# Performance work log

Hardware: AMD Instinct MI355X
Metric: run time of the kernel (lower is better)

Reference implementation:

```python
import math
import jax, jax.numpy as jnp
import numpy as np

# ---------------- static structure (mirrors CG_woFilter_cuda + MyBatchNormWeightMM) ----------------
LMAX = 4
TAUS = [16, 16, 16, 16, 16]          # t_F: input channels per degree l
T_O  = [16, 16, 16, 16, 16]          # output channels per degree l after weight matmul
BN_EPS = 1e-5

# all (l, l1, l2) triples with l2 <= l1 <= lmax and |l1-l2| <= l <= min(l1+l2, lmax), sorted by (l,l1,l2)
TRIPLES = sorted([(l, l1, l2)
                  for l1 in range(LMAX + 1)
                  for l2 in range(l1 + 1)
                  for l in range(l1 - l2, min(l1 + l2, LMAX) + 1)])

T_FF = [0] * (LMAX + 1)              # t_FF[l] = sum over triples of taus[l1]*taus[l2]
for (l, l1, l2) in TRIPLES:
    T_FF[l] += TAUS[l1] * TAUS[l2]

def _cg_coef(j1, m1, j2, m2, j, m):
    """Clebsch-Gordan coefficient <j1 m1 j2 m2 | j m> (Condon-Shortley)."""
    if m1 + m2 != m:
        return 0.0
    f = math.factorial
    if j < abs(j1 - j2) or j > j1 + j2:
        return 0.0
    pref = math.sqrt((2 * j + 1) * f(j + j1 - j2) * f(j - j1 + j2) * f(j1 + j2 - j) / f(j1 + j2 + j + 1))
    pref *= math.sqrt(f(j + m) * f(j - m) * f(j1 - m1) * f(j1 + m1) * f(j2 - m2) * f(j2 + m2))
    s = 0.0
    for k in range(0, j1 + j2 - j + 1):
        if (j1 - m1 - k) < 0 or (j2 + m2 - k) < 0 or (j - j2 + m1 + k) < 0 or (j - j1 - m2 + k) < 0:
            continue
        s += ((-1.0) ** k) / (f(k) * f(j1 + j2 - j - k) * f(j1 - m1 - k)
                              * f(j2 + m2 - k) * f(j - j2 + m1 + k) * f(j - j1 - m2 + k))
    return pref * s

def _cg_matrix(l, l1, l2):
    C = np.zeros((2 * l + 1, 2 * l1 + 1, 2 * l2 + 1), dtype=np.float32)
    for m in range(-l, l + 1):
        for m1 in range(-l1, l1 + 1):
            m2 = m - m1
            if -l2 <= m2 <= l2:
                C[m + l, m1 + l1, m2 + l2] = _cg_coef(l1, m1, l2, m2, l, m)
    return C

CG_MATS = {t: jnp.asarray(_cg_matrix(*t)) for t in TRIPLES}

M_IN = sum(TAUS[l] * (2 * l + 1) for l in range(LMAX + 1))      # 400
W_LEN = sum(T_FF[l] * T_O[l] for l in range(LMAX + 1))          # 172032


def setup_inputs() -> dict:
    key = jax.random.key(0)
    k1, k2 = jax.random.split(key)
    B = 256
    Fs = jax.random.normal(k1, (B, M_IN, 2), dtype=jnp.float32)
    W = jax.random.normal(k2, (W_LEN, 2), dtype=jnp.float32) * 0.05
    return {"Fs": Fs, "W": W}


def reference(Fs, W):
    B = Fs.shape[0]
    # split input into per-degree blocks: F_l [B, tau, 2l+1, 2]
    Fl, off = [], 0
    for l in range(LMAX + 1):
        n = TAUS[l] * (2 * l + 1)
        Fl.append(Fs[:, off:off + n, :].reshape(B, TAUS[l], 2 * l + 1, 2))
        off += n
    # sparse CG tensor product: per-triple complex outer product contracted with CG coefs
    frags = [[] for _ in range(LMAX + 1)]
    for (l, l1, l2) in TRIPLES:
        C = CG_MATS[(l, l1, l2)]                     # [2l+1, 2l1+1, 2l2+1]
        a, b = Fl[l1], Fl[l2]
        ar, ai = a[..., 0], a[..., 1]
        br, bi = b[..., 0], b[..., 1]
        rr = jnp.einsum('bip,bjq,mpq->bijm', ar, br, C)
        ii = jnp.einsum('bip,bjq,mpq->bijm', ai, bi, C)
        ri = jnp.einsum('bip,bjq,mpq->bijm', ar, bi, C)
        ir = jnp.einsum('bip,bjq,mpq->bijm', ai, br, C)
        fr = (rr - ii).reshape(B, -1, 2 * l + 1)     # channels flattened as c1*tau2 + c2 (t_offsets order)
        fi = (ri + ir).reshape(B, -1, 2 * l + 1)
        frags[l].append(jnp.stack([fr, fi], axis=-1))
    # per-degree fragment batchnorm + complex weight matmul (FN_WMM)
    outs, woff = [], 0
    for l in range(LMAX + 1):
        FF = jnp.concatenate(frags[l], axis=1)       # [B, t_FF, 2l+1, 2]
        var = jnp.mean(jnp.sum(FF * FF, axis=-1), axis=(0, 2))      # per-channel mean |z|^2
        FFn = FF / (jnp.sqrt(var)[None, :, None, None] + BN_EPS)
        n = T_FF[l] * T_O[l]
        Wl = W[woff:woff + n].reshape(T_O[l], T_FF[l], 2)
        woff += n
        wr, wi = Wl[..., 0], Wl[..., 1]
        xr, xi = FFn[..., 0], FFn[..., 1]
        yr = jnp.einsum('oc,bcm->bom', wr, xr) - jnp.einsum('oc,bcm->bom', wi, xi)
        yi = jnp.einsum('oc,bcm->bom', wr, xi) + jnp.einsum('oc,bcm->bom', wi, xr)
        outs.append(jnp.stack([yr, yi], axis=-1).reshape(B, T_O[l] * (2 * l + 1), 2))
    return jnp.concatenate(outs, axis=1)             # [B, sum t_O[l]*(2l+1), 2] = [B, 400, 2]
```

## Files before the change

kernel.cpp:

```cpp
#include <hip/hip_runtime.h>
#include <math.h>

#define NTRI 42
#define NCH  10752
#define B_SZ 256
#define AH_PL 172032

typedef float    f32x4 __attribute__((ext_vector_type(4)));
typedef _Float16 half8 __attribute__((ext_vector_type(8)));
typedef _Float16 half4 __attribute__((ext_vector_type(4)));
typedef _Float16 f16x2 __attribute__((ext_vector_type(2)));

constexpr int CT_L [NTRI]={0,0,0,0,0, 1,1,1,1,1,1,1,1, 2,2,2,2,2,2,2,2,2,2, 3,3,3,3,3,3,3,3,3,3, 4,4,4,4,4,4,4,4,4};
constexpr int CT_L1[NTRI]={0,1,2,3,4, 1,1,2,2,3,3,4,4, 1,2,2,2,3,3,3,4,4,4, 2,2,3,3,3,3,4,4,4,4, 2,3,3,3,4,4,4,4,4};
constexpr int CT_L2[NTRI]={0,1,2,3,4, 0,1,1,2,2,3,3,4, 1,0,1,2,1,2,3,2,3,4, 1,2,0,1,2,3,1,2,3,4, 2,1,2,3,0,1,2,3,4};
constexpr int CT_T [NTRI]={0,1,2,3,4, 0,1,2,3,4,5,6,7, 0,1,2,3,4,5,6,7,8,9, 0,1,2,3,4,5,6,7,8,9, 0,1,2,3,4,5,6,7,8};

constexpr int KL_t[5]    ={1280,2048,2560,2560,2304};
constexpr int GBASE_t[5] ={0,1280,3328,5888,8448};
constexpr int ROFF_t[5]  ={0,16,64,144,256};
constexpr int NM_t[5]    ={1,3,5,7,9};
constexpr int FFB_t[5]   ={0,327680,1900544,5177344,9764864};
#define FF_TOT 15073280
constexpr int PL_t[5]    ={0,5,29,79,149};
#define PART_PL 4096
#define PART_TOT (230*PART_PL)

__device__ const int   dCTL[NTRI]={0,0,0,0,0, 1,1,1,1,1,1,1,1, 2,2,2,2,2,2,2,2,2,2, 3,3,3,3,3,3,3,3,3,3, 4,4,4,4,4,4,4,4,4};
__device__ const int   dCTT[NTRI]={0,1,2,3,4, 0,1,2,3,4,5,6,7, 0,1,2,3,4,5,6,7,8,9, 0,1,2,3,4,5,6,7,8,9, 0,1,2,3,4,5,6,7,8};
__device__ const int   dK[5]   ={1280,2048,2560,2560,2304};
__device__ const int   dWOFF[5]={0,20480,53248,94208,135168};
__device__ const int   dNM[5]  ={1,3,5,7,9};
__device__ const int   dFFB[5] ={0,327680,1900544,5177344,9764864};
__device__ const int   dPL[5]  ={0,5,29,79,149};
__device__ const int   dGB[5]  ={0,1280,3328,5888,8448};
__device__ const int   dROFF[5]={0,16,64,144,256};
__device__ const int   dNT[5]  ={5,8,10,10,9};
__device__ const float dINV[5] ={1.f/256.f,1.f/768.f,1.f/1280.f,1.f/1792.f,1.f/2304.f};

__device__ float  g_varsum[NCH];
__device__ __align__(16) f16x2  g_ff[FF_TOT];
__device__ __align__(16) f16x2  g_ah[2*AH_PL];
__device__ float2 g_part[PART_TOT];

constexpr double cfact(int n){ double r=1.0; for(int i=2;i<=n;i++) r*=(double)i; return r; }
constexpr double csqrt_(double v){ double x = v>1.0? v:1.0; for(int i=0;i<80;i++) x = 0.5*(x+v/x); return x; }
constexpr double ccg(int j1,int m1,int j2,int m2,int j,int m){
    if(m1+m2!=m) return 0.0;
    double pref = csqrt_((2.0*j+1.0)*cfact(j+j1-j2)*cfact(j-j1+j2)*cfact(j1+j2-j)/cfact(j1+j2+j+1));
    pref *= csqrt_(cfact(j+m)*cfact(j-m)*cfact(j1-m1)*cfact(j1+m1)*cfact(j2-m2)*cfact(j2+m2));
    double s=0.0;
    for(int k=0;k<=j1+j2-j;k++){
        int a=j1-m1-k, bb=j2+m2-k, c=j-j2+m1+k, d=j-j1-m2+k;
        if(a<0||bb<0||c<0||d<0) continue;
        double term = 1.0/(cfact(k)*cfact(j1+j2-j-k)*cfact(a)*cfact(bb)*cfact(c)*cfact(d));
        s += (k&1)? -term : term;
    }
    return pref*s;
}
struct CG81 { float a[81]; };
constexpr CG81 makecg(int l,int l1,int l2){
    CG81 t{};
    const int n1=2*l1+1;
    for(int mi=0;mi<2*l+1;mi++)
        for(int p=0;p<n1;p++){
            const int m=mi-l, m1=p-l1, m2=m-m1;
            if(m2>=-l2 && m2<=l2) t.a[mi*n1+p]=(float)ccg(l1,m1,l2,m2,l,m);
        }
    return t;
}
template<int TR> struct CGC { static constexpr CG81 t = makecg(CT_L[TR],CT_L1[TR],CT_L2[TR]); };

template<int TR>
__device__ __forceinline__ void cg_pair(const float2* __restrict__ sF,
                                        int i, int j0,
                                        float2* __restrict__ ff0,
                                        float2* __restrict__ ff1){
    constexpr int L=CT_L[TR], L1=CT_L1[TR], L2=CT_L2[TR];
    constexpr int N1=2*L1+1, N2=2*L2+1, NM=2*L+1;
    float2 A[N1], B0[N2], B1[N2];
    #pragma unroll
    for(int p=0;p<N1;p++) A[p]=sF[ROFF_t[L1]+i*N1+p];
    #pragma unroll
    for(int q=0;q<N2;q++) B0[q]=sF[ROFF_t[L2]+j0*N2+q];
    #pragma unroll
    for(int q=0;q<N2;q++) B1[q]=sF[ROFF_t[L2]+(j0+1)*N2+q];
    #pragma unroll
    for(int mi=0;mi<NM;mi++){
        float aR0=0.f, aI0=0.f, aR1=0.f, aI1=0.f;
        const int pLo = (mi-L+L1-L2) > 0 ? (mi-L+L1-L2) : 0;
        const int pHi = (mi-L+L1+L2) < 2*L1 ? (mi-L+L1+L2) : 2*L1;
        #pragma unroll
        for(int p=0;p<N1;p++){
            if(p>=pLo && p<=pHi){
                const float c = CGC<TR>::t.a[mi*N1+p];
                if(c != 0.f){
                    const int q = mi - L - p + L1 + L2;
                    const float2 a=A[p];
                    const float2 b0=B0[q], b1=B1[q];
                    aR0 = fmaf(c, a.x*b0.x - a.y*b0.y, aR0);
                    aI0 = fmaf(c, a.x*b0.y + a.y*b0.x, aI0);
                    aR1 = fmaf(c, a.x*b1.x - a.y*b1.y, aR1);
                    aI1 = fmaf(c, a.x*b1.y + a.y*b1.x, aI1);
                }
            }
        }
        ff0[mi]=make_float2(aR0,aI0);
        ff1[mi]=make_float2(aR1,aI1);
    }
}

template<int TR>
__device__ __forceinline__ void cg_one(const float2* __restrict__ sF, int bq, int t){
    constexpr int L=CT_L[TR], NM=2*L+1, T=CT_T[TR], K=KL_t[L];
    constexpr int NMK=NM*K;
    const int half = t>>7, tt = t&127;
    const int ch0 = tt*2;
    const int i = ch0>>4, j0 = ch0&15;
    float n20=0.f, n21=0.f;
    #pragma unroll
    for(int b4=0;b4<4;b4++){
        const int slab = half*4+b4;
        const int b = bq*8 + slab;
        float2 ff0[NM], ff1[NM];
        cg_pair<TR>(sF + slab*400, i, j0, ff0, ff1);
        const int base = FFB_t[L] + b*NMK + T*256 + ch0;
        #pragma unroll
        for(int m=0;m<NM;m++){
            n20 = fmaf(ff0[m].x,ff0[m].x,n20); n20 = fmaf(ff0[m].y,ff0[m].y,n20);
            n21 = fmaf(ff1[m].x,ff1[m].x,n21); n21 = fmaf(ff1[m].y,ff1[m].y,n21);
            half4 h;
            h[0]=(_Float16)ff0[m].x; h[1]=(_Float16)ff0[m].y;
            h[2]=(_Float16)ff1[m].x; h[3]=(_Float16)ff1[m].y;
            *reinterpret_cast<half4*>(g_ff + base + m*K) = h;
        }
    }
    atomicAdd(&g_varsum[GBASE_t[L] + T*256 + ch0    ], n20);
    atomicAdd(&g_varsum[GBASE_t[L] + T*256 + ch0 + 1], n21);
}

template<int TR>
__device__ __forceinline__ void cg_disp(int tr, const float2* sF, int bq, int t){
    if constexpr (TR < NTRI){
        if(tr==TR) cg_one<TR>(sF,bq,t);
        else       cg_disp<TR+1>(tr,sF,bq,t);
    }
}

__global__ void __launch_bounds__(256) k_cg(const float2* __restrict__ Fs){
    __shared__ float4 sF4[1600];
    const int bq=blockIdx.y, t=threadIdx.x;
    const float4* __restrict__ F4 = reinterpret_cast<const float4*>(Fs) + bq*1600;
    #pragma unroll
    for(int k=0;k<6;k++) sF4[t + k*256] = F4[t + k*256];
    if(t<64) sF4[t+1536] = F4[t+1536];
    __syncthreads();
    cg_disp<0>(blockIdx.x, reinterpret_cast<const float2*>(sF4), bq, t);
}

__global__ void __launch_bounds__(256) k_wn(const float2* __restrict__ W2){
    const int tr=blockIdx.x, t=threadIdx.x;
    const int l=dCTL[tr], T=dCTT[tr], K=dK[l];
    const float s = g_varsum[dGB[l] + T*256 + t];
    const float invv = 1.f/(sqrtf(s*dINV[l])+1e-5f);
    const int base = dWOFF[l] + T*256 + t;
    #pragma unroll 4
    for(int o=0;o<16;o++){
        const float2 w = W2[base + o*K];
        f16x2 hr, hi;
        hr.x=(_Float16)( w.x*invv); hr.y=(_Float16)(-w.y*invv);
        hi.x=(_Float16)( w.y*invv); hi.y=(_Float16)( w.x*invv);
        g_ah[base + o*K]         = hr;
        g_ah[AH_PL + base + o*K] = hi;
    }
}

__global__ void __launch_bounds__(256) k_mm(){
    const int j=blockIdx.x;
    const int wv=threadIdx.x>>6, lane=threadIdx.x&63;
    const int slot=blockIdx.y*4+wv;
    const int bgA=slot, bgB=slot+8;
    const int l=(j<5)?0:(j<29)?1:(j<79)?2:(j<149)?3:4;
    const int nm=dNM[l];
    const int loc=j-dPL[l];
    const int T=loc/nm, m=loc-T*nm;
    const int K=dK[l];
    const int l15=lane&15, kg=lane>>4;
    const half8* __restrict__ Arp = reinterpret_cast<const half8*>(g_ah + dWOFF[l] + l15*K + T*256 + kg*4);
    const half8* __restrict__ Aip = reinterpret_cast<const half8*>(g_ah + AH_PL + dWOFF[l] + l15*K + T*256 + kg*4);
    const half8* __restrict__ XpA = reinterpret_cast<const half8*>(g_ff + dFFB[l] + (bgA*16+l15)*(nm*K) + m*K + T*256 + kg*4);
    const half8* __restrict__ XpB = reinterpret_cast<const half8*>(g_ff + dFFB[l] + (bgB*16+l15)*(nm*K) + m*K + T*256 + kg*4);
    f32x4 arA={0.f,0.f,0.f,0.f}, aiA={0.f,0.f,0.f,0.f};
    f32x4 arB={0.f,0.f,0.f,0.f}, aiB={0.f,0.f,0.f,0.f};
    #pragma unroll
    for(int ks=0; ks<16; ks++){
        const half8 Ar = Arp[ks*4];
        const half8 Ai = Aip[ks*4];
        const half8 BA = XpA[ks*4];
        const half8 BB = XpB[ks*4];
        arA = __builtin_amdgcn_mfma_f32_16x16x32_f16(Ar, BA, arA, 0,0,0);
        aiA = __builtin_amdgcn_mfma_f32_16x16x32_f16(Ai, BA, aiA, 0,0,0);
        arB = __builtin_amdgcn_mfma_f32_16x16x32_f16(Ar, BB, arB, 0,0,0);
        aiB = __builtin_amdgcn_mfma_f32_16x16x32_f16(Ai, BB, aiB, 0,0,0);
    }
    float2* __restrict__ ppA = g_part + j*PART_PL + bgA*256;
    float2* __restrict__ ppB = g_part + j*PART_PL + bgB*256;
    #pragma unroll
    for(int r=0;r<4;r++){
        ppA[(kg*4+r)*16 + l15] = make_float2(arA[r], aiA[r]);
        ppB[(kg*4+r)*16 + l15] = make_float2(arB[r], aiB[r]);
    }
}

__global__ void __launch_bounds__(448) k_red(float2* __restrict__ out){
    const int b=blockIdx.x, r=threadIdx.x;
    if(r>=400) return;
    const int l = (r<16)?0:(r<64)?1:(r<144)?2:(r<256)?3:4;
    const int om = r - dROFF[l];
    const int nm = dNM[l];
    const int o = om/nm, m = om - o*nm;
    const float2* __restrict__ pp = g_part + (dPL[l]+m)*PART_PL + (b>>4)*256 + o*16 + (b&15);
    float2 s=make_float2(0.f,0.f);
    const int nt=dNT[l];
    for(int T=0;T<nt;T++){
        const float2 v = pp[T*nm*PART_PL];
        s.x+=v.x; s.y+=v.y;
    }
    out[b*400+r]=s;
}

extern "C" void kernel_launch(void* const* d_in, const int* in_sizes, int n_in,
                              void* d_out, int out_size, void* d_ws, size_t ws_size,
                              hipStream_t stream){
    const float2* Fs = (const float2*)d_in[0];
    const float2* W  = (const float2*)d_in[1];
    float2* out = (float2*)d_out;

    void* dvs=nullptr;
    hipGetSymbolAddress(&dvs, HIP_SYMBOL(g_varsum));
    hipMemsetAsync(dvs, 0, NCH*sizeof(float), stream);

    k_cg <<<dim3(NTRI,32), 256, 0, stream>>>(Fs);
    k_wn <<<dim3(NTRI),    256, 0, stream>>>(W);
    k_mm <<<dim3(230,2),   256, 0, stream>>>();
    k_red<<<dim3(B_SZ),    448, 0, stream>>>(out);
}
```

Measured before the change: 116.5 us.

## Register-block CG products over four j-channels and drop varsum memset

Each thread in the CG kernel now computes four output channels (one i, four consecutive j) for two batch slabs, instead of two channels for four slabs. This reuses the A vector and the CG coefficient products across four B vectors and writes half8 stores. The hipMemsetAsync of the variance accumulator is removed; k_wn now zeroes each entry after reading it, which relies on the buffer starting at zero on the first call. The trade-offs are more register pressure from the B arrays and a non-unrolled slab loop.

```diff
diff --git a/kernel.cpp b/kernel.cpp
--- a/kernel.cpp
+++ b/kernel.cpp
@@ -72,71 +72,63 @@
 template<int TR> struct CGC { static constexpr CG81 t = makecg(CT_L[TR],CT_L1[TR],CT_L2[TR]); };
 
 template<int TR>
-__device__ __forceinline__ void cg_pair(const float2* __restrict__ sF,
-                                        int i, int j0,
-                                        float2* __restrict__ ff0,
-                                        float2* __restrict__ ff1){
+__device__ __forceinline__ void cg_one(const float2* __restrict__ sF, int bq, int t){
     constexpr int L=CT_L[TR], L1=CT_L1[TR], L2=CT_L2[TR];
     constexpr int N1=2*L1+1, N2=2*L2+1, NM=2*L+1;
-    float2 A[N1], B0[N2], B1[N2];
-    #pragma unroll
-    for(int p=0;p<N1;p++) A[p]=sF[ROFF_t[L1]+i*N1+p];
-    #pragma unroll
-    for(int q=0;q<N2;q++) B0[q]=sF[ROFF_t[L2]+j0*N2+q];
-    #pragma unroll
-    for(int q=0;q<N2;q++) B1[q]=sF[ROFF_t[L2]+(j0+1)*N2+q];
-    #pragma unroll
-    for(int mi=0;mi<NM;mi++){
-        float aR0=0.f, aI0=0.f, aR1=0.f, aI1=0.f;
-        const int pLo = (mi-L+L1-L2) > 0 ? (mi-L+L1-L2) : 0;
-        const int pHi = (mi-L+L1+L2) < 2*L1 ? (mi-L+L1+L2) : 2*L1;
+    constexpr int T=CT_T[TR], K=KL_t[L], NMK=NM*K;
+    const int q = t&63, sg = t>>6;
+    const int i = q>>2, j0 = (q&3)*4, ch0 = q*4;
+    float n2[4]={0.f,0.f,0.f,0.f};
+    #pragma unroll 1
+    for(int b2=0;b2<2;b2++){
+        const int slab = sg*2+b2;
+        const int b = bq*8+slab;
+        const float2* __restrict__ sFb = sF + slab*400;
+        float2 A[N1];
         #pragma unroll
-        for(int p=0;p<N1;p++){
-            if(p>=pLo && p<=pHi){
-                const float c = CGC<TR>::t.a[mi*N1+p];
-                if(c != 0.f){
-                    const int q = mi - L - p + L1 + L2;
-                    const float2 a=A[p];
-                    const float2 b0=B0[q], b1=B1[q];
-                    aR0 = fmaf(c, a.x*b0.x - a.y*b0.y, aR0);
-                    aI0 = fmaf(c, a.x*b0.y + a.y*b0.x, aI0);
-                    aR1 = fmaf(c, a.x*b1.x - a.y*b1.y, aR1);
-                    aI1 = fmaf(c, a.x*b1.y + a.y*b1.x, aI1);
+        for(int p=0;p<N1;p++) A[p]=sFb[ROFF_t[L1]+i*N1+p];
+        float2 Bv[4][N2];
+        #pragma unroll
+        for(int jj=0;jj<4;jj++){
+            #pragma unroll
+            for(int qq=0;qq<N2;qq++) Bv[jj][qq]=sFb[ROFF_t[L2]+(j0+jj)*N2+qq];
+        }
+        const int base = FFB_t[L] + b*NMK + T*256 + ch0;
+        #pragma unroll
+        for(int mi=0;mi<NM;mi++){
+            float aR[4]={0.f,0.f,0.f,0.f}, aI[4]={0.f,0.f,0.f,0.f};
+            const int pLo = (mi-L+L1-L2) > 0 ? (mi-L+L1-L2) : 0;
+            const int pHi = (mi-L+L1+L2) < 2*L1 ? (mi-L+L1+L2) : 2*L1;
+            #pragma unroll
+            for(int p=0;p<N1;p++){
+                if(p>=pLo && p<=pHi){
+                    const float c = CGC<TR>::t.a[mi*N1+p];
+                    if(c != 0.f){
+                        const int qq = mi - L - p + L1 + L2;
+                        const float cax=c*A[p].x, cay=c*A[p].y;
+                        #pragma unroll
+                        for(int jj=0;jj<4;jj++){
+                            const float2 bb=Bv[jj][qq];
+                            aR[jj]=fmaf(cax,bb.x,aR[jj]); aR[jj]=fmaf(-cay,bb.y,aR[jj]);
+                            aI[jj]=fmaf(cax,bb.y,aI[jj]); aI[jj]=fmaf( cay,bb.x,aI[jj]);
+                        }
+                    }
                 }
             }
+            half8 h;
+            #pragma unroll
+            for(int jj=0;jj<4;jj++){
+                n2[jj]=fmaf(aR[jj],aR[jj],n2[jj]);
+                n2[jj]=fmaf(aI[jj],aI[jj],n2[jj]);
+                h[2*jj]  =(_Float16)aR[jj];
+                h[2*jj+1]=(_Float16)aI[jj];
+            }
+            *reinterpret_cast<half8*>(g_ff + base + mi*K) = h;
         }
-        ff0[mi]=make_float2(aR0,aI0);
-        ff1[mi]=make_float2(aR1,aI1);
-    }
-}
-
-template<int TR>
-__device__ __forceinline__ void cg_one(const float2* __restrict__ sF, int bq, int t){
-    constexpr int L=CT_L[TR], NM=2*L+1, T=CT_T[TR], K=KL_t[L];
-    constexpr int NMK=NM*K;
-    const int half = t>>7, tt = t&127;
-    const int ch0 = tt*2;
-    const int i = ch0>>4, j0 = ch0&15;
-    float n20=0.f, n21=0.f;
-    #pragma unroll
-    for(int b4=0;b4<4;b4++){
-        const int slab = half*4+b4;
-        const int b = bq*8 + slab;
-        float2 ff0[NM], ff1[NM];
-        cg_pair<TR>(sF + slab*400, i, j0, ff0, ff1);
-        const int base = FFB_t[L] + b*NMK + T*256 + ch0;
-        #pragma unroll
-        for(int m=0;m<NM;m++){
-            n20 = fmaf(ff0[m].x,ff0[m].x,n20); n20 = fmaf(ff0[m].y,ff0[m].y,n20);
-            n21 = fmaf(ff1[m].x,ff1[m].x,n21); n21 = fmaf(ff1[m].y,ff1[m].y,n21);
-            half4 h;
-            h[0]=(_Float16)ff0[m].x; h[1]=(_Float16)ff0[m].y;
-            h[2]=(_Float16)ff1[m].x; h[3]=(_Float16)ff1[m].y;
-            *reinterpret_cast<half4*>(g_ff + base + m*K) = h;
-        }
-    }
-    atomicAdd(&g_varsum[GBASE_t[L] + T*256 + ch0    ], n20);
-    atomicAdd(&g_varsum[GBASE_t[L] + T*256 + ch0 + 1], n21);
+    }
+    #pragma unroll
+    for(int jj=0;jj<4;jj++)
+        atomicAdd(&g_varsum[GBASE_t[L] + T*256 + ch0 + jj], n2[jj]);
 }
 
 template<int TR>
@@ -161,7 +153,9 @@
 __global__ void __launch_bounds__(256) k_wn(const float2* __restrict__ W2){
     const int tr=blockIdx.x, t=threadIdx.x;
     const int l=dCTL[tr], T=dCTT[tr], K=dK[l];
-    const float s = g_varsum[dGB[l] + T*256 + t];
+    const int ch = dGB[l] + T*256 + t;
+    const float s = g_varsum[ch];
+    g_varsum[ch] = 0.f;
     const float invv = 1.f/(sqrtf(s*dINV[l])+1e-5f);
     const int base = dWOFF[l] + T*256 + t;
     #pragma unroll 4
@@ -236,10 +230,6 @@
     const float2* W  = (const float2*)d_in[1];
     float2* out = (float2*)d_out;
 
-    void* dvs=nullptr;
-    hipGetSymbolAddress(&dvs, HIP_SYMBOL(g_varsum));
-    hipMemsetAsync(dvs, 0, NCH*sizeof(float), stream);
-
     k_cg <<<dim3(NTRI,32), 256, 0, stream>>>(Fs);
     k_wn <<<dim3(NTRI),    256, 0, stream>>>(W);
     k_mm <<<dim3(230,2),   256, 0, stream>>>();
```

Measured after the change: 130.8 us. 12.3% more time.
